# Kernel tuning notes

Measured on AMD Instinct MI355X. Metric: run time of the kernel, lower is better.

The kernel has to match this reference:

```python
import jax, jax.numpy as jnp
import numpy as np

B, T, F, H, V = 256, 1024, 64, 32, 13


def setup_inputs() -> dict:
    key = jax.random.key(0)
    ks = jax.random.split(key, 6)
    s = 0.05
    return {
        "x": jax.random.normal(ks[0], (B, T, F), dtype=jnp.float32),
        "W": jax.random.normal(ks[1], (F, 4 * H), dtype=jnp.float32) * s,   # input kernel (Keras order i,f,c,o)
        "U": jax.random.normal(ks[2], (H, 4 * H), dtype=jnp.float32) * s,   # recurrent kernel
        "b": jnp.zeros((4 * H,), dtype=jnp.float32),                        # bias
        "Wd": jax.random.normal(ks[3], (H, V), dtype=jnp.float32) * s,      # TimeDistributed Dense kernel
        "bd": jnp.zeros((V,), dtype=jnp.float32),
    }


def _lstm(x, W, U, b):
    # Precompute input projections for all timesteps: [B,T,4H]
    xz = jnp.einsum("btf,fk->btk", x, W) + b
    h0 = jnp.zeros((x.shape[0], H), dtype=x.dtype)
    c0 = jnp.zeros((x.shape[0], H), dtype=x.dtype)

    def step(carry, xz_t):
        h, c = carry
        z = xz_t + h @ U                      # [B,4H]
        i = jax.nn.sigmoid(z[:, 0 * H:1 * H])
        f = jax.nn.sigmoid(z[:, 1 * H:2 * H])
        g = jnp.tanh(z[:, 2 * H:3 * H])
        o = jax.nn.sigmoid(z[:, 3 * H:4 * H])
        c_new = f * c + i * g
        h_new = o * jnp.tanh(c_new)
        return (h_new, c_new), h_new

    _, hs = jax.lax.scan(step, (h0, c0), jnp.swapaxes(xz, 0, 1))  # hs: [T,B,H]
    return jnp.swapaxes(hs, 0, 1)                                  # [B,T,H]


def reference(x, W, U, b, Wd, bd):
    h = _lstm(x, W, U, b)                                  # [B,T,H]
    logits = jnp.einsum("bth,hv->btv", h, Wd) + bd         # [B,T,V]
    return jax.nn.softmax(logits, axis=-1)
```

## Files before the change

### kernel.cpp

```cpp
#include <hip/hip_runtime.h>

#define B_ 256
#define T_ 1024
#define F_ 64
#define H_ 32
#define V_ 13
#define K4 128

__device__ __forceinline__ void fma4(float4& acc, float s, const float4& wv) {
  acc.x = fmaf(s, wv.x, acc.x);
  acc.y = fmaf(s, wv.y, acc.y);
  acc.z = fmaf(s, wv.z, acc.z);
  acc.w = fmaf(s, wv.w, acc.w);
}

__global__ __launch_bounds__(256, 2) void xz_gemm(const float* __restrict__ x,
                                                  const float* __restrict__ W,
                                                  const float* __restrict__ bias,
                                                  float* __restrict__ xz) {
  __shared__ float4 Ws4[F_ * 32];
  __shared__ float4 Xs4[128 * 16];

  const float4* W4 = (const float4*)W;
  for (int i = threadIdx.x; i < F_ * 32; i += 256) Ws4[i] = W4[i];
  const int row0 = blockIdx.x * 128;
  const float4* X4 = (const float4*)(x + (size_t)row0 * F_);
  for (int i = threadIdx.x; i < 128 * 16; i += 256) Xs4[i] = X4[i];
  __syncthreads();

  const int cg = threadIdx.x & 31;
  const int rs = threadIdx.x >> 5;
  const float4 bv = ((const float4*)bias)[cg];

  float4 acc[16];
#pragma unroll
  for (int rr = 0; rr < 16; ++rr) acc[rr] = bv;

#pragma unroll
  for (int fg = 0; fg < 16; ++fg) {
    float4 w0 = Ws4[(4 * fg + 0) * 32 + cg];
    float4 w1 = Ws4[(4 * fg + 1) * 32 + cg];
    float4 w2 = Ws4[(4 * fg + 2) * 32 + cg];
    float4 w3 = Ws4[(4 * fg + 3) * 32 + cg];
#pragma unroll
    for (int rr = 0; rr < 16; ++rr) {
      float4 xv = Xs4[(rs + 8 * rr) * 16 + fg];
      fma4(acc[rr], xv.x, w0);
      fma4(acc[rr], xv.y, w1);
      fma4(acc[rr], xv.z, w2);
      fma4(acc[rr], xv.w, w3);
    }
  }
#pragma unroll
  for (int rr = 0; rr < 16; ++rr) {
    ((float4*)(xz + (size_t)(row0 + rs + 8 * rr) * K4))[cg] = acc[rr];
  }
}

__device__ __forceinline__ float sigmoid_(float x) { return 1.f / (1.f + __expf(-x)); }
__device__ __forceinline__ float tanh_(float x)    { return 1.f - 2.f / (__expf(2.f * x) + 1.f); }
__device__ __forceinline__ float bcast_(float v, int j) {
  return __uint_as_float(__builtin_amdgcn_readlane(__float_as_uint(v), j));
}

__global__ __launch_bounds__(64) void lstm_scan(float* __restrict__ zbuf,
                                                const float* __restrict__ U) {
  const int lane = threadIdx.x;
  const int kA = lane;
  const int kB = lane + 64;
  float Ua[H_], Ub[H_];
#pragma unroll
  for (int j = 0; j < H_; ++j) {
    Ua[j] = U[j * K4 + kA];
    Ub[j] = U[j * K4 + kB];
  }
  float* zb = zbuf + (size_t)blockIdx.x * T_ * K4;

  float qa0 = zb[(size_t)0 * K4 + kA], qb0 = zb[(size_t)0 * K4 + kB];
  float qa1 = zb[(size_t)1 * K4 + kA], qb1 = zb[(size_t)1 * K4 + kB];
  float qa2 = zb[(size_t)2 * K4 + kA], qb2 = zb[(size_t)2 * K4 + kB];
  float qa3 = zb[(size_t)3 * K4 + kA], qb3 = zb[(size_t)3 * K4 + kB];

  float c = 0.f, hval = 0.f;
  const bool loA = (lane < H_);

  auto step = [&](float& qa, float& qb, int t, int tl) {
    const float zAin = qa, zBin = qb;
    const int tc = (tl < T_) ? tl : (T_ - 1);
    qa = zb[(size_t)tc * K4 + kA];
    qb = zb[(size_t)tc * K4 + kB];

    float a0 = zAin, a1 = 0.f, a2 = 0.f, a3 = 0.f;
    float b0 = zBin, b1 = 0.f, b2 = 0.f, b3 = 0.f;
#pragma unroll
    for (int j = 0; j < H_; j += 4) {
      float h0 = bcast_(hval, j + 0);
      float h1 = bcast_(hval, j + 1);
      float h2 = bcast_(hval, j + 2);
      float h3 = bcast_(hval, j + 3);
      a0 = fmaf(h0, Ua[j + 0], a0);  b0 = fmaf(h0, Ub[j + 0], b0);
      a1 = fmaf(h1, Ua[j + 1], a1);  b1 = fmaf(h1, Ub[j + 1], b1);
      a2 = fmaf(h2, Ua[j + 2], a2);  b2 = fmaf(h2, Ub[j + 2], b2);
      a3 = fmaf(h3, Ua[j + 3], a3);  b3 = fmaf(h3, Ub[j + 3], b3);
    }
    const float zA = (a0 + a1) + (a2 + a3);
    const float zB = (b0 + b1) + (b2 + b3);

    const float rA = __shfl_xor(zA, 32);
    const float rB = __shfl_xor(zB, 32);
    const float iv = loA ? zA : rA;
    const float fv = loA ? rA : zA;
    const float gv = loA ? zB : rB;
    const float ov = loA ? rB : zB;

    const float ig = sigmoid_(iv);
    const float fg = sigmoid_(fv);
    const float gg = tanh_(gv);
    const float og = sigmoid_(ov);
    c = fmaf(fg, c, ig * gg);
    hval = og * tanh_(c);

    if (loA) zb[(size_t)t * K4 + lane] = hval;
  };

  for (int t = 0; t < T_; t += 4) {
    step(qa0, qb0, t + 0, t + 4);
    step(qa1, qb1, t + 1, t + 5);
    step(qa2, qb2, t + 2, t + 6);
    step(qa3, qb3, t + 3, t + 7);
  }
}

__global__ __launch_bounds__(256) void dense_softmax(const float* __restrict__ hbuf,
                                                     const float* __restrict__ Wd,
                                                     const float* __restrict__ bd,
                                                     float* __restrict__ out) {
  __shared__ float4 Wds4[H_ * 4];
  __shared__ float  bds[16];
  if (threadIdx.x < 128) {
    const int j = threadIdx.x >> 2, q = threadIdx.x & 3;
    float4 v = make_float4(0.f, 0.f, 0.f, 0.f);
    const int c0 = q * 4;
    if (c0 + 0 < V_) v.x = Wd[j * V_ + c0 + 0];
    if (c0 + 1 < V_) v.y = Wd[j * V_ + c0 + 1];
    if (c0 + 2 < V_) v.z = Wd[j * V_ + c0 + 2];
    if (c0 + 3 < V_) v.w = Wd[j * V_ + c0 + 3];
    Wds4[j * 4 + q] = v;
  }
  if (threadIdx.x < 16) bds[threadIdx.x] = (threadIdx.x < V_) ? bd[threadIdx.x] : 0.f;
  __syncthreads();

  const int row = blockIdx.x * 256 + threadIdx.x;
  const float4* hr = (const float4*)(hbuf + (size_t)row * K4);
  float h[H_];
#pragma unroll
  for (int j = 0; j < H_ / 4; ++j) {
    float4 v = hr[j];
    h[4 * j + 0] = v.x; h[4 * j + 1] = v.y; h[4 * j + 2] = v.z; h[4 * j + 3] = v.w;
  }
  float4 acc[4];
#pragma unroll
  for (int q = 0; q < 4; ++q)
    acc[q] = make_float4(bds[4 * q], bds[4 * q + 1], bds[4 * q + 2], bds[4 * q + 3]);
#pragma unroll
  for (int j = 0; j < H_; ++j) {
    const float hj = h[j];
    fma4(acc[0], hj, Wds4[j * 4 + 0]);
    fma4(acc[1], hj, Wds4[j * 4 + 1]);
    fma4(acc[2], hj, Wds4[j * 4 + 2]);
    fma4(acc[3], hj, Wds4[j * 4 + 3]);
  }
  float lg[16];
#pragma unroll
  for (int q = 0; q < 4; ++q) {
    lg[4 * q + 0] = acc[q].x; lg[4 * q + 1] = acc[q].y;
    lg[4 * q + 2] = acc[q].z; lg[4 * q + 3] = acc[q].w;
  }
  float m = lg[0];
#pragma unroll
  for (int v = 1; v < V_; ++v) m = fmaxf(m, lg[v]);
  float s = 0.f;
#pragma unroll
  for (int v = 0; v < V_; ++v) { float e = __expf(lg[v] - m); lg[v] = e; s += e; }
  const float r = 1.f / s;
  float* orow = out + (size_t)row * V_;
#pragma unroll
  for (int v = 0; v < V_; ++v) orow[v] = lg[v] * r;
}

extern "C" void kernel_launch(void* const* d_in, const int* in_sizes, int n_in,
                              void* d_out, int out_size, void* d_ws, size_t ws_size,
                              hipStream_t stream) {
  const float* x  = (const float*)d_in[0];
  const float* W  = (const float*)d_in[1];
  const float* U  = (const float*)d_in[2];
  const float* b  = (const float*)d_in[3];
  const float* Wd = (const float*)d_in[4];
  const float* bd = (const float*)d_in[5];
  float* out  = (float*)d_out;
  float* zbuf = (float*)d_ws;

  xz_gemm<<<(B_ * T_) / 128, 256, 0, stream>>>(x, W, b, zbuf);
  lstm_scan<<<B_, 64, 0, stream>>>(zbuf, U);
  dense_softmax<<<(B_ * T_) / 256, 256, 0, stream>>>(zbuf, Wd, bd, out);
}
```

Measured before the change: 529.3 us.

## Compute LSTM recurrent matmul with split-fp16 MFMA and four waves per block

The per-step h@U recurrence moves from scalar FMAs with readlane broadcasts to 16x16x32 f16 MFMA instructions. Both h and U are split into high and scaled-low fp16 parts so that three MFMAs approximate fp32 accuracy. h is distributed to lanes via ds_bpermute. Blocks now hold four batch waves, with the occupancy hint set to one wave per EU. The aim is to shorten the serial per-step latency of the scan, at the cost of MFMA latency on the critical path and a small precision risk.

```diff
diff --git a/kernel.cpp b/kernel.cpp
--- a/kernel.cpp
+++ b/kernel.cpp
@@ -6,6 +6,11 @@
 #define H_ 32
 #define V_ 13
 #define K4 128
+
+typedef _Float16 f16x8 __attribute__((ext_vector_type(8)));
+typedef __fp16   fp16x2 __attribute__((ext_vector_type(2)));
+typedef float    f32x4 __attribute__((ext_vector_type(4)));
+typedef unsigned int u32x4 __attribute__((ext_vector_type(4)));
 
 __device__ __forceinline__ void fma4(float4& acc, float s, const float4& wv) {
   acc.x = fmaf(s, wv.x, acc.x);
@@ -59,75 +64,105 @@
 
 __device__ __forceinline__ float sigmoid_(float x) { return 1.f / (1.f + __expf(-x)); }
 __device__ __forceinline__ float tanh_(float x)    { return 1.f - 2.f / (__expf(2.f * x) + 1.f); }
-__device__ __forceinline__ float bcast_(float v, int j) {
-  return __uint_as_float(__builtin_amdgcn_readlane(__float_as_uint(v), j));
-}
-
-__global__ __launch_bounds__(64) void lstm_scan(float* __restrict__ zbuf,
-                                                const float* __restrict__ U) {
-  const int lane = threadIdx.x;
-  const int kA = lane;
-  const int kB = lane + 64;
-  float Ua[H_], Ub[H_];
-#pragma unroll
-  for (int j = 0; j < H_; ++j) {
-    Ua[j] = U[j * K4 + kA];
-    Ub[j] = U[j * K4 + kB];
-  }
-  float* zb = zbuf + (size_t)blockIdx.x * T_ * K4;
-
-  float qa0 = zb[(size_t)0 * K4 + kA], qb0 = zb[(size_t)0 * K4 + kB];
-  float qa1 = zb[(size_t)1 * K4 + kA], qb1 = zb[(size_t)1 * K4 + kB];
-  float qa2 = zb[(size_t)2 * K4 + kA], qb2 = zb[(size_t)2 * K4 + kB];
-  float qa3 = zb[(size_t)3 * K4 + kA], qb3 = zb[(size_t)3 * K4 + kB];
-
-  float c = 0.f, hval = 0.f;
-  const bool loA = (lane < H_);
-
-  auto step = [&](float& qa, float& qb, int t, int tl) {
-    const float zAin = qa, zBin = qb;
+
+__global__ __launch_bounds__(256)
+__attribute__((amdgpu_waves_per_eu(1, 1)))
+void lstm_scan(float* __restrict__ zbuf, const float* __restrict__ U) {
+  const int lane = threadIdx.x & 63;
+  const int wv   = threadIdx.x >> 6;
+  const int batch = blockIdx.x * 4 + wv;
+  const int g = lane >> 4;
+  const int m = lane & 15;
+
+  f16x8 ufh[8], ufl[8];
+#pragma unroll
+  for (int c = 0; c < 8; ++c) {
+    const int col = 32 * (c >> 1) + 2 * m + (c & 1);
+#pragma unroll
+    for (int e = 0; e < 8; ++e) {
+      const float u = U[(8 * g + e) * K4 + col];
+      const _Float16 uh = (_Float16)u;
+      ufh[c][e] = uh;
+      ufl[c][e] = (_Float16)((u - (float)uh) * 2048.0f);
+    }
+  }
+  asm volatile("" : "+v"(ufh[0]), "+v"(ufh[1]), "+v"(ufh[2]), "+v"(ufh[3]),
+                    "+v"(ufh[4]), "+v"(ufh[5]), "+v"(ufh[6]), "+v"(ufh[7]));
+  asm volatile("" : "+v"(ufl[0]), "+v"(ufl[1]), "+v"(ufl[2]), "+v"(ufl[3]),
+                    "+v"(ufl[4]), "+v"(ufl[5]), "+v"(ufl[6]), "+v"(ufl[7]));
+
+  float* zb = zbuf + (size_t)batch * T_ * K4;
+  const float* xp = zb + 2 * m;
+
+  float2 pre[4][4];
+#pragma unroll
+  for (int s = 0; s < 4; ++s)
+#pragma unroll
+    for (int a = 0; a < 4; ++a)
+      pre[s][a] = *(const float2*)(xp + s * K4 + 32 * a);
+
+  const int bpa = 16 * g;
+  int hph = 0, hpl = 0;
+  float c0 = 0.f, c1 = 0.f;
+  const f32x4 zz = {0.f, 0.f, 0.f, 0.f};
+  const bool st = (lane < 16);
+
+  auto step = [&](float2 (&pr)[4], int t, int tl) {
+    u32x4 bh, bl;
+    bh.x = __builtin_amdgcn_ds_bpermute(bpa + 0,  hph);
+    bh.y = __builtin_amdgcn_ds_bpermute(bpa + 4,  hph);
+    bh.z = __builtin_amdgcn_ds_bpermute(bpa + 8,  hph);
+    bh.w = __builtin_amdgcn_ds_bpermute(bpa + 12, hph);
+    bl.x = __builtin_amdgcn_ds_bpermute(bpa + 0,  hpl);
+    bl.y = __builtin_amdgcn_ds_bpermute(bpa + 4,  hpl);
+    bl.z = __builtin_amdgcn_ds_bpermute(bpa + 8,  hpl);
+    bl.w = __builtin_amdgcn_ds_bpermute(bpa + 12, hpl);
+    const f16x8 afh = __builtin_bit_cast(f16x8, bh);
+    const f16x8 afl = __builtin_bit_cast(f16x8, bl);
+
+    float z[8];
+#pragma unroll
+    for (int a = 0; a < 4; ++a) {
+#pragma unroll
+      for (int p = 0; p < 2; ++p) {
+        const int cc = 2 * a + p;
+        f32x4 mn = __builtin_amdgcn_mfma_f32_16x16x32_f16(afh, ufh[cc], zz, 0, 0, 0);
+        f32x4 cr = __builtin_amdgcn_mfma_f32_16x16x32_f16(afh, ufl[cc], zz, 0, 0, 0);
+        cr = __builtin_amdgcn_mfma_f32_16x16x32_f16(afl, ufh[cc], cr, 0, 0, 0);
+        const float xzv = p ? pr[a].y : pr[a].x;
+        z[cc] = fmaf(cr[0], 4.8828125e-4f, mn[0] + xzv);
+      }
+    }
+
     const int tc = (tl < T_) ? tl : (T_ - 1);
-    qa = zb[(size_t)tc * K4 + kA];
-    qb = zb[(size_t)tc * K4 + kB];
-
-    float a0 = zAin, a1 = 0.f, a2 = 0.f, a3 = 0.f;
-    float b0 = zBin, b1 = 0.f, b2 = 0.f, b3 = 0.f;
-#pragma unroll
-    for (int j = 0; j < H_; j += 4) {
-      float h0 = bcast_(hval, j + 0);
-      float h1 = bcast_(hval, j + 1);
-      float h2 = bcast_(hval, j + 2);
-      float h3 = bcast_(hval, j + 3);
-      a0 = fmaf(h0, Ua[j + 0], a0);  b0 = fmaf(h0, Ub[j + 0], b0);
-      a1 = fmaf(h1, Ua[j + 1], a1);  b1 = fmaf(h1, Ub[j + 1], b1);
-      a2 = fmaf(h2, Ua[j + 2], a2);  b2 = fmaf(h2, Ub[j + 2], b2);
-      a3 = fmaf(h3, Ua[j + 3], a3);  b3 = fmaf(h3, Ub[j + 3], b3);
-    }
-    const float zA = (a0 + a1) + (a2 + a3);
-    const float zB = (b0 + b1) + (b2 + b3);
-
-    const float rA = __shfl_xor(zA, 32);
-    const float rB = __shfl_xor(zB, 32);
-    const float iv = loA ? zA : rA;
-    const float fv = loA ? rA : zA;
-    const float gv = loA ? zB : rB;
-    const float ov = loA ? rB : zB;
-
-    const float ig = sigmoid_(iv);
-    const float fg = sigmoid_(fv);
-    const float gg = tanh_(gv);
-    const float og = sigmoid_(ov);
-    c = fmaf(fg, c, ig * gg);
-    hval = og * tanh_(c);
-
-    if (loA) zb[(size_t)t * K4 + lane] = hval;
+    const float* xq = xp + (size_t)tc * K4;
+#pragma unroll
+    for (int a = 0; a < 4; ++a) pr[a] = *(const float2*)(xq + 32 * a);
+
+    const float i0 = sigmoid_(z[0]), i1 = sigmoid_(z[1]);
+    const float f0 = sigmoid_(z[2]), f1 = sigmoid_(z[3]);
+    const float g0 = tanh_(z[4]),    g1 = tanh_(z[5]);
+    const float o0 = sigmoid_(z[6]), o1 = sigmoid_(z[7]);
+    c0 = fmaf(f0, c0, i0 * g0);
+    c1 = fmaf(f1, c1, i1 * g1);
+    const float h0 = o0 * tanh_(c0);
+    const float h1 = o1 * tanh_(c1);
+
+    if (st) *(float2*)(zb + (size_t)t * K4 + 2 * m) = make_float2(h0, h1);
+
+    const fp16x2 ph = __builtin_amdgcn_cvt_pkrtz(h0, h1);
+    const float r0 = (h0 - (float)ph[0]) * 2048.0f;
+    const float r1 = (h1 - (float)ph[1]) * 2048.0f;
+    const fp16x2 pl = __builtin_amdgcn_cvt_pkrtz(r0, r1);
+    hph = __builtin_bit_cast(int, ph);
+    hpl = __builtin_bit_cast(int, pl);
   };
 
   for (int t = 0; t < T_; t += 4) {
-    step(qa0, qb0, t + 0, t + 4);
-    step(qa1, qb1, t + 1, t + 5);
-    step(qa2, qb2, t + 2, t + 6);
-    step(qa3, qb3, t + 3, t + 7);
+    step(pre[0], t + 0, t + 4);
+    step(pre[1], t + 1, t + 5);
+    step(pre[2], t + 2, t + 6);
+    step(pre[3], t + 3, t + 7);
   }
 }
 
@@ -176,12 +211,12 @@
     lg[4 * q + 0] = acc[q].x; lg[4 * q + 1] = acc[q].y;
     lg[4 * q + 2] = acc[q].z; lg[4 * q + 3] = acc[q].w;
   }
-  float m = lg[0];
-#pragma unroll
-  for (int v = 1; v < V_; ++v) m = fmaxf(m, lg[v]);
+  float mx = lg[0];
+#pragma unroll
+  for (int v = 1; v < V_; ++v) mx = fmaxf(mx, lg[v]);
   float s = 0.f;
 #pragma unroll
-  for (int v = 0; v < V_; ++v) { float e = __expf(lg[v] - m); lg[v] = e; s += e; }
+  for (int v = 0; v < V_; ++v) { float e = __expf(lg[v] - mx); lg[v] = e; s += e; }
   const float r = 1.f / s;
   float* orow = out + (size_t)row * V_;
 #pragma unroll
@@ -201,6 +236,6 @@
   float* zbuf = (float*)d_ws;
 
   xz_gemm<<<(B_ * T_) / 128, 256, 0, stream>>>(x, W, b, zbuf);
-  lstm_scan<<<B_, 64, 0, stream>>>(zbuf, U);
+  lstm_scan<<<B_ / 4, 256, 0, stream>>>(zbuf, U);
   dense_softmax<<<(B_ * T_) / 256, 256, 0, stream>>>(zbuf, Wd, bd, out);
 }
```

After: 706.2 us. +33.4%, slower.
